# Performance work log

Hardware: AMD Instinct MI355X
Metric: run time of the kernel (lower is better)

The kernel has to match this reference:

```python
import jax, jax.numpy as jnp
import numpy as np
import math

H = 16
EPS = 1e-5

def _layernorm(x, g, b):
    mu = jnp.mean(x, axis=-1, keepdims=True)
    var = jnp.var(x, axis=-1, keepdims=True)
    return (x - mu) * jax.lax.rsqrt(var + EPS) * g + b

def setup_inputs() -> dict:
    key = jax.random.key(0)
    ks = jax.random.split(key, 8)
    B, S, D, F, M = 2, 2048, 1024, 4096, 64
    dh = D // H
    s = 1.0 / math.sqrt(D)
    return {
        "x": jax.random.normal(ks[0], (B, S, D), jnp.float32),
        "Wq": jax.random.normal(ks[1], (D, D), jnp.float32) * s,
        "Wk": jax.random.normal(ks[2], (D, D), jnp.float32) * s,
        "Wv": jax.random.normal(ks[3], (D, D), jnp.float32) * s,
        "Wo": jax.random.normal(ks[4], (D, D), jnp.float32) * s,
        "Mk": jax.random.normal(ks[5], (H, dh, M), jnp.float32) / math.sqrt(dh),
        "ln1_g": jnp.ones((D,), jnp.float32),
        "ln1_b": jnp.zeros((D,), jnp.float32),
        "ln2_g": jnp.ones((D,), jnp.float32),
        "ln2_b": jnp.zeros((D,), jnp.float32),
        "W1": jax.random.normal(ks[6], (D, F), jnp.float32) * s,
        "b1": jnp.zeros((F,), jnp.float32),
        "W2": jax.random.normal(ks[7], (F, D), jnp.float32) / math.sqrt(F),
        "b2": jnp.zeros((D,), jnp.float32),
    }

def reference(x, Wq, Wk, Wv, Wo, Mk, ln1_g, ln1_b, ln2_g, ln2_b, W1, b1, W2, b2):
    B, S, D = x.shape
    dh = D // H
    def split(t):  # (B,S,D) -> (B,H,S,dh)
        return t.reshape(B, S, H, dh).transpose(0, 2, 1, 3)
    qh = split(x @ Wq)
    kh = split(x @ Wk)
    vh = split(x @ Wv)
    q_mem = jnp.einsum('bhsd,hdm->bhsm', qh, Mk)
    k_mem = jnp.einsum('bhsd,hdm->bhsm', kh, Mk)
    attn = jnp.einsum('bhsm,bhtm->bhst', q_mem, k_mem) / math.sqrt(dh)
    attn = jax.nn.softmax(attn, axis=-1)
    ctx = jnp.einsum('bhst,bhtd->bhsd', attn, vh)
    ctx = ctx.transpose(0, 2, 1, 3).reshape(B, S, D)
    x = _layernorm(x + ctx @ Wo, ln1_g, ln1_b)
    ff = jax.nn.gelu(x @ W1 + b1, approximate=False) @ W2 + b2
    return _layernorm(x + ff, ln2_g, ln2_b)
```

## Files before the change

### kernel.cpp

```cpp
#include <hip/hip_runtime.h>
#include <math.h>

#define NH 16
#define DH 64
#define MDIM 64
#define DMODEL 1024
#define FDIM 4096
#define BATCH 2
#define SEQ 2048
#define NROWS (BATCH*SEQ)

typedef short bf16x8 __attribute__((ext_vector_type(8)));
typedef float f32x4 __attribute__((ext_vector_type(4)));

__device__ __forceinline__ float gelu_f(float v) {
    return 0.5f * v * (1.0f + erff(v * 0.70710678118654752f));
}
__device__ __forceinline__ ushort f2bf(float f) {
    union { float f; unsigned u; } v; v.f = f;
    unsigned r = v.u + 0x7fffu + ((v.u >> 16) & 1u);
    return (ushort)(r >> 16);
}
__device__ __forceinline__ float bf2f(ushort h) {
    union { unsigned u; float f; } v; v.u = ((unsigned)h) << 16;
    return v.f;
}
__device__ __forceinline__ void gl_lds16(const ushort* g, ushort* l) {
    __builtin_amdgcn_global_load_lds((const __attribute__((address_space(1))) void*)g,
                                     (__attribute__((address_space(3))) void*)l, 16, 0, 0);
}

__global__ __launch_bounds__(256)
void splitA_kernel(const float* __restrict__ X, ushort* __restrict__ hi,
                   ushort* __restrict__ lo, int n4) {
    int i = blockIdx.x * 256 + threadIdx.x;
    if (i >= n4) return;
    float4 v = ((const float4*)X)[i];
    ushort4 h, l;
    h.x = f2bf(v.x); l.x = f2bf(v.x - bf2f(h.x));
    h.y = f2bf(v.y); l.y = f2bf(v.y - bf2f(h.y));
    h.z = f2bf(v.z); l.z = f2bf(v.z - bf2f(h.z));
    h.w = f2bf(v.w); l.w = f2bf(v.w - bf2f(h.w));
    ((ushort4*)hi)[i] = h;
    ((ushort4*)lo)[i] = l;
}

__global__ __launch_bounds__(256)
void splitT_kernel(const float* __restrict__ W, ushort* __restrict__ Thi,
                   ushort* __restrict__ Tlo, int K, int N) {
    __shared__ float tile[64][65];
    const int n0 = blockIdx.x * 64;
    const int k0 = blockIdx.y * 64;
    const int t  = threadIdx.x;
    const int r  = t >> 4;
    const int c4 = (t & 15) * 4;
#pragma unroll
    for (int i = 0; i < 4; ++i) {
        int row = r + i * 16;
        float4 v = *(const float4*)&W[(size_t)(k0 + row) * N + n0 + c4];
        tile[c4 + 0][row] = v.x;
        tile[c4 + 1][row] = v.y;
        tile[c4 + 2][row] = v.z;
        tile[c4 + 3][row] = v.w;
    }
    __syncthreads();
#pragma unroll
    for (int i = 0; i < 4; ++i) {
        int row = r + i * 16;
        float a = tile[row][c4 + 0], b = tile[row][c4 + 1];
        float c = tile[row][c4 + 2], d = tile[row][c4 + 3];
        ushort4 h, l;
        h.x = f2bf(a); l.x = f2bf(a - bf2f(h.x));
        h.y = f2bf(b); l.y = f2bf(b - bf2f(h.y));
        h.z = f2bf(c); l.z = f2bf(c - bf2f(h.z));
        h.w = f2bf(d); l.w = f2bf(d - bf2f(h.w));
        size_t off = (size_t)(n0 + row) * K + k0 + c4;
        *(ushort4*)&Thi[off] = h;
        *(ushort4*)&Tlo[off] = l;
    }
}

template<int ACT, int SPLIT_OUT>
__global__ __launch_bounds__(256)
void mfma_gemm(const ushort* __restrict__ Ahi, const ushort* __restrict__ Alo,
               const ushort* __restrict__ BThi, const ushort* __restrict__ BTlo,
               const float* __restrict__ bias, float* __restrict__ C,
               ushort* __restrict__ Chi, ushort* __restrict__ Clo,
               int K, int N) {
    __shared__ ushort As[128 * 32];
    __shared__ ushort Bs[128 * 32];
    const int t    = threadIdx.x;
    const int lane = t & 63;
    const int wid  = t >> 6;
    const int wr   = wid >> 1;
    const int wc   = wid & 1;
    const int i0   = blockIdx.y * 128;
    const int n0   = blockIdx.x * 128;
    const int srow = t >> 2;
    const int scol = (t & 3) * 8;
    ushort* aDst0 = As + t * 8;
    ushort* aDst1 = As + 2048 + t * 8;
    ushort* bDst0 = Bs + t * 8;
    ushort* bDst1 = Bs + 2048 + t * 8;

    f32x4 acc[4][4];
#pragma unroll
    for (int m = 0; m < 4; ++m)
#pragma unroll
        for (int n = 0; n < 4; ++n) {
            acc[m][n][0] = 0.f; acc[m][n][1] = 0.f;
            acc[m][n][2] = 0.f; acc[m][n][3] = 0.f;
        }

    const int aOff = (wr * 64 + (lane & 15)) * 32 + (lane >> 4) * 8;
    const int bOff = (wc * 64 + (lane & 15)) * 32 + (lane >> 4) * 8;

    for (int seg = 0; seg < 3; ++seg) {
        const ushort* Ab = (seg == 1) ? Alo : Ahi;
        const ushort* Bb = (seg == 2) ? BTlo : BThi;
        const ushort* Ap0 = Ab + (size_t)(i0 + srow) * K + scol;
        const ushort* Ap1 = Ap0 + (size_t)64 * K;
        const ushort* Bp0 = Bb + (size_t)(n0 + srow) * K + scol;
        const ushort* Bp1 = Bp0 + (size_t)64 * K;
        for (int k0 = 0; k0 < K; k0 += 32) {
            __syncthreads();
            gl_lds16(Ap0 + k0, aDst0);
            gl_lds16(Ap1 + k0, aDst1);
            gl_lds16(Bp0 + k0, bDst0);
            gl_lds16(Bp1 + k0, bDst1);
            __syncthreads();
            bf16x8 af[4], bfr[4];
#pragma unroll
            for (int m = 0; m < 4; ++m)
                af[m] = *(const bf16x8*)&As[aOff + m * 16 * 32];
#pragma unroll
            for (int n = 0; n < 4; ++n)
                bfr[n] = *(const bf16x8*)&Bs[bOff + n * 16 * 32];
#pragma unroll
            for (int m = 0; m < 4; ++m)
#pragma unroll
                for (int n = 0; n < 4; ++n)
                    acc[m][n] = __builtin_amdgcn_mfma_f32_16x16x32_bf16(af[m], bfr[n], acc[m][n], 0, 0, 0);
        }
    }

    const int orow  = i0 + wr * 64 + (lane >> 4) * 4;
    const int ocol0 = n0 + wc * 64 + (lane & 15);
#pragma unroll
    for (int n = 0; n < 4; ++n) {
        const int colg = ocol0 + n * 16;
        float bv = bias ? bias[colg] : 0.f;
#pragma unroll
        for (int m = 0; m < 4; ++m) {
#pragma unroll
            for (int r = 0; r < 4; ++r) {
                const int rowg = orow + m * 16 + r;
                float v = acc[m][n][r] + bv;
                if (ACT == 1) v = gelu_f(v);
                size_t off = (size_t)rowg * N + colg;
                if (SPLIT_OUT) {
                    ushort h = f2bf(v);
                    Chi[off] = h;
                    Clo[off] = f2bf(v - bf2f(h));
                } else {
                    C[off] = v;
                }
            }
        }
    }
}

__global__ __launch_bounds__(256)
void headproj_kernel(const float* __restrict__ X, int xstride, const float* __restrict__ Mk,
                     ushort* __restrict__ oh, ushort* __restrict__ ol) {
    __shared__ float Qs[64][65];
    __shared__ float Ms[64][68];
    const int s0 = blockIdx.x * 64;
    const int h  = blockIdx.y;
    const int b  = blockIdx.z;
    const int t  = threadIdx.x;
    const int tc = t & 15, tr = t >> 4;
    const float* xb = X + (size_t)(b * SEQ + s0) * xstride + h * 64;
    const float* mk = Mk + (size_t)h * 64 * 64;
#pragma unroll
    for (int i = 0; i < 4; ++i) {
        int e4  = t + i * 256;
        int row = e4 >> 4;
        int c4  = (e4 & 15) << 2;
        float4 q4 = *(const float4*)(xb + (size_t)row * xstride + c4);
        Qs[c4 + 0][row] = q4.x;
        Qs[c4 + 1][row] = q4.y;
        Qs[c4 + 2][row] = q4.z;
        Qs[c4 + 3][row] = q4.w;
        float4 m4 = *(const float4*)(mk + row * 64 + c4);
        *(float4*)&Ms[row][c4] = m4;
    }
    __syncthreads();
    float acc[4][4] = {};
#pragma unroll 16
    for (int kk = 0; kk < 64; ++kk) {
        float a0 = Qs[kk][tr * 4 + 0];
        float a1 = Qs[kk][tr * 4 + 1];
        float a2 = Qs[kk][tr * 4 + 2];
        float a3 = Qs[kk][tr * 4 + 3];
        float4 b4 = *(const float4*)&Ms[kk][tc * 4];
        acc[0][0] += a0 * b4.x; acc[0][1] += a0 * b4.y; acc[0][2] += a0 * b4.z; acc[0][3] += a0 * b4.w;
        acc[1][0] += a1 * b4.x; acc[1][1] += a1 * b4.y; acc[1][2] += a1 * b4.z; acc[1][3] += a1 * b4.w;
        acc[2][0] += a2 * b4.x; acc[2][1] += a2 * b4.y; acc[2][2] += a2 * b4.z; acc[2][3] += a2 * b4.w;
        acc[3][0] += a3 * b4.x; acc[3][1] += a3 * b4.y; acc[3][2] += a3 * b4.z; acc[3][3] += a3 * b4.w;
    }
    ushort* oph = oh + ((size_t)(b * NH + h) * SEQ + s0) * 64;
    ushort* opl = ol + ((size_t)(b * NH + h) * SEQ + s0) * 64;
#pragma unroll
    for (int i = 0; i < 4; ++i) {
        ushort4 h4, l4;
        h4.x = f2bf(acc[i][0]); l4.x = f2bf(acc[i][0] - bf2f(h4.x));
        h4.y = f2bf(acc[i][1]); l4.y = f2bf(acc[i][1] - bf2f(h4.y));
        h4.z = f2bf(acc[i][2]); l4.z = f2bf(acc[i][2] - bf2f(h4.z));
        h4.w = f2bf(acc[i][3]); l4.w = f2bf(acc[i][3] - bf2f(h4.w));
        *(ushort4*)(oph + (size_t)(tr * 4 + i) * 64 + tc * 4) = h4;
        *(ushort4*)(opl + (size_t)(tr * 4 + i) * 64 + tc * 4) = l4;
    }
}

__global__ __launch_bounds__(256)
void vsplitT_kernel(const float* __restrict__ qkv, ushort* __restrict__ vth,
                    ushort* __restrict__ vtl) {
    __shared__ float tile[64][65];
    const int s0 = blockIdx.x * 64;
    const int h  = blockIdx.y;
    const int b  = blockIdx.z;
    const int t  = threadIdx.x;
    const int r  = t >> 4;
    const int c4 = (t & 15) * 4;
    const float* src = qkv + (size_t)(b * SEQ + s0) * 3072 + 2048 + h * 64;
#pragma unroll
    for (int i = 0; i < 4; ++i) {
        int srow = r + i * 16;
        float4 v = *(const float4*)(src + (size_t)srow * 3072 + c4);
        tile[c4 + 0][srow] = v.x;
        tile[c4 + 1][srow] = v.y;
        tile[c4 + 2][srow] = v.z;
        tile[c4 + 3][srow] = v.w;
    }
    __syncthreads();
    const size_t obase = (size_t)(b * NH + h) * 64 * SEQ + s0;
#pragma unroll
    for (int i = 0; i < 4; ++i) {
        int d = r + i * 16;
        float a = tile[d][c4 + 0], bb = tile[d][c4 + 1];
        float c = tile[d][c4 + 2], dd = tile[d][c4 + 3];
        ushort4 h4, l4;
        h4.x = f2bf(a);  l4.x = f2bf(a - bf2f(h4.x));
        h4.y = f2bf(bb); l4.y = f2bf(bb - bf2f(h4.y));
        h4.z = f2bf(c);  l4.z = f2bf(c - bf2f(h4.z));
        h4.w = f2bf(dd); l4.w = f2bf(dd - bf2f(h4.w));
        *(ushort4*)&vth[obase + (size_t)d * SEQ + c4] = h4;
        *(ushort4*)&vtl[obase + (size_t)d * SEQ + c4] = l4;
    }
}

__global__ __launch_bounds__(256)
void attn_mfma(const ushort* __restrict__ qmh, const ushort* __restrict__ qml,
               const ushort* __restrict__ kmh, const ushort* __restrict__ kml,
               const ushort* __restrict__ vth, const ushort* __restrict__ vtl,
               ushort* __restrict__ ctx_hi, ushort* __restrict__ ctx_lo) {
    __shared__ ushort pbuf[4][2][1024];
    const int q0 = blockIdx.x * 64;
    const int h  = blockIdx.y;
    const int b  = blockIdx.z;
    const int t  = threadIdx.x;
    const int lane = t & 63;
    const int w  = t >> 6;
    const int rg = lane >> 4;
    const int lc = lane & 15;
    const size_t bh = (size_t)b * NH + h;

    const ushort* qb_h = qmh + (bh * SEQ + q0 + w * 16 + lc) * 64 + rg * 8;
    const ushort* qb_l = qml + (bh * SEQ + q0 + w * 16 + lc) * 64 + rg * 8;
    bf16x8 qfh[2], qfl[2];
    qfh[0] = *(const bf16x8*)(qb_h);
    qfh[1] = *(const bf16x8*)(qb_h + 32);
    qfl[0] = *(const bf16x8*)(qb_l);
    qfl[1] = *(const bf16x8*)(qb_l + 32);

    const ushort* kb_h = kmh + (bh * SEQ + lc) * 64 + rg * 8;
    const ushort* kb_l = kml + (bh * SEQ + lc) * 64 + rg * 8;
    const ushort* vb_h = vth + (bh * 64 + lc) * SEQ + rg * 8;
    const ushort* vb_l = vtl + (bh * 64 + lc) * SEQ + rg * 8;

    f32x4 ctx[4];
#pragma unroll
    for (int n = 0; n < 4; ++n) { ctx[n][0] = 0.f; ctx[n][1] = 0.f; ctx[n][2] = 0.f; ctx[n][3] = 0.f; }
    float m_r[4] = { -INFINITY, -INFINITY, -INFINITY, -INFINITY };
    float l_r[4] = { 0.f, 0.f, 0.f, 0.f };

    ushort* ph = &pbuf[w][0][0];
    ushort* pl = &pbuf[w][1][0];

    for (int kv0 = 0; kv0 < SEQ; kv0 += 64) {
        f32x4 sacc[4];
#pragma unroll
        for (int n = 0; n < 4; ++n) { sacc[n][0] = 0.f; sacc[n][1] = 0.f; sacc[n][2] = 0.f; sacc[n][3] = 0.f; }
        bf16x8 bf[4][2];
#pragma unroll
        for (int n = 0; n < 4; ++n) {
            bf[n][0] = *(const bf16x8*)(kb_h + (size_t)(kv0 + 16 * n) * 64);
            bf[n][1] = *(const bf16x8*)(kb_h + (size_t)(kv0 + 16 * n) * 64 + 32);
        }
#pragma unroll
        for (int n = 0; n < 4; ++n) {
            sacc[n] = __builtin_amdgcn_mfma_f32_16x16x32_bf16(qfh[0], bf[n][0], sacc[n], 0, 0, 0);
            sacc[n] = __builtin_amdgcn_mfma_f32_16x16x32_bf16(qfh[1], bf[n][1], sacc[n], 0, 0, 0);
            sacc[n] = __builtin_amdgcn_mfma_f32_16x16x32_bf16(qfl[0], bf[n][0], sacc[n], 0, 0, 0);
            sacc[n] = __builtin_amdgcn_mfma_f32_16x16x32_bf16(qfl[1], bf[n][1], sacc[n], 0, 0, 0);
        }
#pragma unroll
        for (int n = 0; n < 4; ++n) {
            bf[n][0] = *(const bf16x8*)(kb_l + (size_t)(kv0 + 16 * n) * 64);
            bf[n][1] = *(const bf16x8*)(kb_l + (size_t)(kv0 + 16 * n) * 64 + 32);
        }
#pragma unroll
        for (int n = 0; n < 4; ++n) {
            sacc[n] = __builtin_amdgcn_mfma_f32_16x16x32_bf16(qfh[0], bf[n][0], sacc[n], 0, 0, 0);
            sacc[n] = __builtin_amdgcn_mfma_f32_16x16x32_bf16(qfh[1], bf[n][1], sacc[n], 0, 0, 0);
        }
#pragma unroll
        for (int r = 0; r < 4; ++r) {
            float s0 = sacc[0][r] * 0.125f;
            float s1 = sacc[1][r] * 0.125f;
            float s2 = sacc[2][r] * 0.125f;
            float s3 = sacc[3][r] * 0.125f;
            float pm = fmaxf(fmaxf(s0, s1), fmaxf(s2, s3));
            pm = fmaxf(pm, __shfl_xor(pm, 1));
            pm = fmaxf(pm, __shfl_xor(pm, 2));
            pm = fmaxf(pm, __shfl_xor(pm, 4));
            pm = fmaxf(pm, __shfl_xor(pm, 8));
            float mnew  = fmaxf(m_r[r], pm);
            float alpha = __expf(m_r[r] - mnew);
            m_r[r] = mnew;
            float p0 = __expf(s0 - mnew);
            float p1 = __expf(s1 - mnew);
            float p2 = __expf(s2 - mnew);
            float p3 = __expf(s3 - mnew);
            float rs = p0 + p1 + p2 + p3;
            rs += __shfl_xor(rs, 1);
            rs += __shfl_xor(rs, 2);
            rs += __shfl_xor(rs, 4);
            rs += __shfl_xor(rs, 8);
            l_r[r] = l_r[r] * alpha + rs;
            ctx[0][r] *= alpha; ctx[1][r] *= alpha; ctx[2][r] *= alpha; ctx[3][r] *= alpha;
            const int q = rg * 4 + r;
            const int swz = (q & 7) << 3;
            const int rowb = q * 64;
            ushort hh;
            hh = f2bf(p0); ph[(rowb + lc)      ^ swz] = hh; pl[(rowb + lc)      ^ swz] = f2bf(p0 - bf2f(hh));
            hh = f2bf(p1); ph[(rowb + lc + 16) ^ swz] = hh; pl[(rowb + lc + 16) ^ swz] = f2bf(p1 - bf2f(hh));
            hh = f2bf(p2); ph[(rowb + lc + 32) ^ swz] = hh; pl[(rowb + lc + 32) ^ swz] = f2bf(p2 - bf2f(hh));
            hh = f2bf(p3); ph[(rowb + lc + 48) ^ swz] = hh; pl[(rowb + lc + 48) ^ swz] = f2bf(p3 - bf2f(hh));
        }
        bf16x8 pah[2], pal[2];
        {
            const int swz = (lc & 7) << 3;
            pah[0] = *(const bf16x8*)&ph[(lc * 64 + rg * 8)      ^ swz];
            pah[1] = *(const bf16x8*)&ph[(lc * 64 + rg * 8 + 32) ^ swz];
            pal[0] = *(const bf16x8*)&pl[(lc * 64 + rg * 8)      ^ swz];
            pal[1] = *(const bf16x8*)&pl[(lc * 64 + rg * 8 + 32) ^ swz];
        }
#pragma unroll
        for (int n = 0; n < 4; ++n) {
            bf[n][0] = *(const bf16x8*)(vb_h + (size_t)(16 * n) * SEQ + kv0);
            bf[n][1] = *(const bf16x8*)(vb_h + (size_t)(16 * n) * SEQ + kv0 + 32);
        }
#pragma unroll
        for (int n = 0; n < 4; ++n) {
            ctx[n] = __builtin_amdgcn_mfma_f32_16x16x32_bf16(pah[0], bf[n][0], ctx[n], 0, 0, 0);
            ctx[n] = __builtin_amdgcn_mfma_f32_16x16x32_bf16(pah[1], bf[n][1], ctx[n], 0, 0, 0);
            ctx[n] = __builtin_amdgcn_mfma_f32_16x16x32_bf16(pal[0], bf[n][0], ctx[n], 0, 0, 0);
            ctx[n] = __builtin_amdgcn_mfma_f32_16x16x32_bf16(pal[1], bf[n][1], ctx[n], 0, 0, 0);
        }
#pragma unroll
        for (int n = 0; n < 4; ++n) {
            bf[n][0] = *(const bf16x8*)(vb_l + (size_t)(16 * n) * SEQ + kv0);
            bf[n][1] = *(const bf16x8*)(vb_l + (size_t)(16 * n) * SEQ + kv0 + 32);
        }
#pragma unroll
        for (int n = 0; n < 4; ++n) {
            ctx[n] = __builtin_amdgcn_mfma_f32_16x16x32_bf16(pah[0], bf[n][0], ctx[n], 0, 0, 0);
            ctx[n] = __builtin_amdgcn_mfma_f32_16x16x32_bf16(pah[1], bf[n][1], ctx[n], 0, 0, 0);
        }
    }
#pragma unroll
    for (int r = 0; r < 4; ++r) {
        float inv = 1.0f / l_r[r];
        const int q = q0 + w * 16 + rg * 4 + r;
        size_t base = ((size_t)b * SEQ + q) * DMODEL + h * 64 + lc;
#pragma unroll
        for (int n = 0; n < 4; ++n) {
            float o = ctx[n][r] * inv;
            ushort hh = f2bf(o);
            ctx_hi[base + 16 * n] = hh;
            ctx_lo[base + 16 * n] = f2bf(o - bf2f(hh));
        }
    }
}

__global__ __launch_bounds__(256)
void ln_kernel(const float* __restrict__ X, const float* __restrict__ R,
               const float* __restrict__ gw, const float* __restrict__ bw,
               float* __restrict__ out, ushort* __restrict__ ohi, ushort* __restrict__ olo) {
    __shared__ float red[8];
    const int i = blockIdx.x;
    const int t = threadIdx.x;
    const float* xp = X + (size_t)i * DMODEL;
    const float* rp = R + (size_t)i * DMODEL;
    float4 xv = *(const float4*)(xp + t * 4);
    float4 rv = *(const float4*)(rp + t * 4);
    float v0 = xv.x + rv.x, v1 = xv.y + rv.y, v2 = xv.z + rv.z, v3 = xv.w + rv.w;
    float sum = v0 + v1 + v2 + v3;
    float sq  = v0 * v0 + v1 * v1 + v2 * v2 + v3 * v3;
#pragma unroll
    for (int off = 32; off > 0; off >>= 1) {
        sum += __shfl_down(sum, off, 64);
        sq  += __shfl_down(sq,  off, 64);
    }
    int wid = t >> 6;
    if ((t & 63) == 0) { red[wid] = sum; red[4 + wid] = sq; }
    __syncthreads();
    sum = red[0] + red[1] + red[2] + red[3];
    sq  = red[4] + red[5] + red[6] + red[7];
    float mu   = sum * (1.0f / DMODEL);
    float var  = sq * (1.0f / DMODEL) - mu * mu;
    float rstd = rsqrtf(var + 1e-5f);
    float4 gv = *(const float4*)(gw + t * 4);
    float4 bv = *(const float4*)(bw + t * 4);
    float4 o;
    o.x = (v0 - mu) * rstd * gv.x + bv.x;
    o.y = (v1 - mu) * rstd * gv.y + bv.y;
    o.z = (v2 - mu) * rstd * gv.z + bv.z;
    o.w = (v3 - mu) * rstd * gv.w + bv.w;
    *(float4*)(out + (size_t)i * DMODEL + t * 4) = o;
    if (ohi) {
        ushort4 h, l;
        h.x = f2bf(o.x); l.x = f2bf(o.x - bf2f(h.x));
        h.y = f2bf(o.y); l.y = f2bf(o.y - bf2f(h.y));
        h.z = f2bf(o.z); l.z = f2bf(o.z - bf2f(h.z));
        h.w = f2bf(o.w); l.w = f2bf(o.w - bf2f(h.w));
        size_t off = (size_t)i * DMODEL + t * 4;
        *(ushort4*)&ohi[off] = h;
        *(ushort4*)&olo[off] = l;
    }
}

extern "C" void kernel_launch(void* const* d_in, const int* in_sizes, int n_in,
                              void* d_out, int out_size, void* d_ws, size_t ws_size,
                              hipStream_t stream) {
    const float* x   = (const float*)d_in[0];
    const float* Wq  = (const float*)d_in[1];
    const float* Wk  = (const float*)d_in[2];
    const float* Wv  = (const float*)d_in[3];
    const float* Wo  = (const float*)d_in[4];
    const float* Mk  = (const float*)d_in[5];
    const float* g1  = (const float*)d_in[6];
    const float* bl1 = (const float*)d_in[7];
    const float* g2  = (const float*)d_in[8];
    const float* bl2 = (const float*)d_in[9];
    const float* W1  = (const float*)d_in[10];
    const float* bf1 = (const float*)d_in[11];
    const float* W2  = (const float*)d_in[12];
    const float* bf2 = (const float*)d_in[13];
    float* out = (float*)d_out;
    char* wsb  = (char*)d_ws;

    const size_t MB = 1024 * 1024;
    float*  qkv   = (float*)(wsb + 0 * MB);
    ushort* qmh   = (ushort*)(wsb + 48 * MB);
    ushort* qml   = (ushort*)(wsb + 56 * MB);
    ushort* kmh   = (ushort*)(wsb + 64 * MB);
    ushort* kml   = (ushort*)(wsb + 72 * MB);
    ushort* vth   = (ushort*)(wsb + 80 * MB);
    ushort* vtl   = (ushort*)(wsb + 88 * MB);
    ushort* x_hi  = (ushort*)(wsb + 96 * MB);
    ushort* x_lo  = (ushort*)(wsb + 104 * MB);
    ushort* ctx_hi = x_hi;
    ushort* ctx_lo = x_lo;
    float*  wo_out = (float*)(wsb + 112 * MB);
    float*  ff2    = wo_out;
    float*  y      = (float*)(wsb + 128 * MB);
    ushort* y_hi   = (ushort*)(wsb + 144 * MB);
    ushort* y_lo   = (ushort*)(wsb + 152 * MB);
    ushort* wqkvT_hi = (ushort*)(wsb + 160 * MB);
    ushort* wqkvT_lo = (ushort*)(wsb + 166 * MB);
    ushort* woT_hi   = (ushort*)(wsb + 172 * MB);
    ushort* woT_lo   = (ushort*)(wsb + 174 * MB);
    ushort* w1T_hi   = (ushort*)(wsb + 176 * MB);
    ushort* w1T_lo   = (ushort*)(wsb + 184 * MB);
    ushort* w2T_hi   = (ushort*)(wsb + 64 * MB);
    ushort* w2T_lo   = (ushort*)(wsb + 72 * MB);
    ushort* h1_hi    = (ushort*)(wsb + 0 * MB);
    ushort* h1_lo    = (ushort*)(wsb + 32 * MB);

    dim3 blk(256);
    dim3 hgrid(SEQ / 64, NH, BATCH);
    splitT_kernel<<<dim3(16, 16), blk, 0, stream>>>(Wq, wqkvT_hi, wqkvT_lo, DMODEL, DMODEL);
    splitT_kernel<<<dim3(16, 16), blk, 0, stream>>>(Wk, wqkvT_hi + (size_t)1024 * 1024, wqkvT_lo + (size_t)1024 * 1024, DMODEL, DMODEL);
    splitT_kernel<<<dim3(16, 16), blk, 0, stream>>>(Wv, wqkvT_hi + (size_t)2048 * 1024, wqkvT_lo + (size_t)2048 * 1024, DMODEL, DMODEL);
    splitT_kernel<<<dim3(16, 16), blk, 0, stream>>>(Wo, woT_hi, woT_lo, DMODEL, DMODEL);
    splitT_kernel<<<dim3(64, 16), blk, 0, stream>>>(W1, w1T_hi, w1T_lo, DMODEL, FDIM);
    splitA_kernel<<<dim3(4096), blk, 0, stream>>>(x, x_hi, x_lo, NROWS * DMODEL / 4);
    mfma_gemm<0, 0><<<dim3(24, 32), blk, 0, stream>>>(x_hi, x_lo, wqkvT_hi, wqkvT_lo,
                                                      nullptr, qkv, nullptr, nullptr, DMODEL, 3072);
    headproj_kernel<<<hgrid, blk, 0, stream>>>(qkv + 0,    3072, Mk, qmh, qml);
    headproj_kernel<<<hgrid, blk, 0, stream>>>(qkv + 1024, 3072, Mk, kmh, kml);
    vsplitT_kernel<<<hgrid, blk, 0, stream>>>(qkv, vth, vtl);
    attn_mfma<<<hgrid, blk, 0, stream>>>(qmh, qml, kmh, kml, vth, vtl, ctx_hi, ctx_lo);
    splitT_kernel<<<dim3(16, 64), blk, 0, stream>>>(W2, w2T_hi, w2T_lo, FDIM, DMODEL);
    mfma_gemm<0, 0><<<dim3(8, 32), blk, 0, stream>>>(ctx_hi, ctx_lo, woT_hi, woT_lo,
                                                     nullptr, wo_out, nullptr, nullptr, DMODEL, DMODEL);
    ln_kernel<<<dim3(NROWS), blk, 0, stream>>>(x, wo_out, g1, bl1, y, y_hi, y_lo);
    mfma_gemm<1, 1><<<dim3(32, 32), blk, 0, stream>>>(y_hi, y_lo, w1T_hi, w1T_lo,
                                                      bf1, nullptr, h1_hi, h1_lo, DMODEL, FDIM);
    mfma_gemm<0, 0><<<dim3(8, 32), blk, 0, stream>>>(h1_hi, h1_lo, w2T_hi, w2T_lo,
                                                     bf2, ff2, nullptr, nullptr, FDIM, DMODEL);
    ln_kernel<<<dim3(NROWS), blk, 0, stream>>>(y, ff2, g2, bl2, out, nullptr, nullptr);
}
```

Measured before the change: 1.256 ms.

## Use single-wave attention blocks with register prefetch of next K tile

The attention kernel now launches one 64-thread wavefront per block, each handling 16 query rows, so the grid has four times as many blocks. Inside the KV loop the next K hi/lo tile is prefetched into registers while the current one is consumed, and V loads are issued earlier so they overlap the softmax. This aims to hide global-memory latency and raise occupancy, at the cost of more live registers and smaller blocks with less shared scheduling.

```diff
diff --git a/kernel.cpp b/kernel.cpp
--- a/kernel.cpp
+++ b/kernel.cpp
@@ -260,24 +260,23 @@
     }
 }
 
-__global__ __launch_bounds__(256)
+__global__ __launch_bounds__(64)
 void attn_mfma(const ushort* __restrict__ qmh, const ushort* __restrict__ qml,
                const ushort* __restrict__ kmh, const ushort* __restrict__ kml,
                const ushort* __restrict__ vth, const ushort* __restrict__ vtl,
                ushort* __restrict__ ctx_hi, ushort* __restrict__ ctx_lo) {
-    __shared__ ushort pbuf[4][2][1024];
-    const int q0 = blockIdx.x * 64;
+    __shared__ ushort ph[1024];
+    __shared__ ushort pl[1024];
+    const int q0 = blockIdx.x * 16;
     const int h  = blockIdx.y;
     const int b  = blockIdx.z;
-    const int t  = threadIdx.x;
-    const int lane = t & 63;
-    const int w  = t >> 6;
+    const int lane = threadIdx.x;
     const int rg = lane >> 4;
     const int lc = lane & 15;
     const size_t bh = (size_t)b * NH + h;
 
-    const ushort* qb_h = qmh + (bh * SEQ + q0 + w * 16 + lc) * 64 + rg * 8;
-    const ushort* qb_l = qml + (bh * SEQ + q0 + w * 16 + lc) * 64 + rg * 8;
+    const ushort* qb_h = qmh + (bh * SEQ + q0 + lc) * 64 + rg * 8;
+    const ushort* qb_l = qml + (bh * SEQ + q0 + lc) * 64 + rg * 8;
     bf16x8 qfh[2], qfl[2];
     qfh[0] = *(const bf16x8*)(qb_h);
     qfh[1] = *(const bf16x8*)(qb_h + 32);
@@ -295,35 +294,43 @@
     float m_r[4] = { -INFINITY, -INFINITY, -INFINITY, -INFINITY };
     float l_r[4] = { 0.f, 0.f, 0.f, 0.f };
 
-    ushort* ph = &pbuf[w][0][0];
-    ushort* pl = &pbuf[w][1][0];
+    bf16x8 kh[4][2], kl[4][2];
+#pragma unroll
+    for (int n = 0; n < 4; ++n) {
+        kh[n][0] = *(const bf16x8*)(kb_h + (size_t)(16 * n) * 64);
+        kh[n][1] = *(const bf16x8*)(kb_h + (size_t)(16 * n) * 64 + 32);
+        kl[n][0] = *(const bf16x8*)(kb_l + (size_t)(16 * n) * 64);
+        kl[n][1] = *(const bf16x8*)(kb_l + (size_t)(16 * n) * 64 + 32);
+    }
 
     for (int kv0 = 0; kv0 < SEQ; kv0 += 64) {
+        bf16x8 vh[4][2];
+#pragma unroll
+        for (int n = 0; n < 4; ++n) {
+            vh[n][0] = *(const bf16x8*)(vb_h + (size_t)(16 * n) * SEQ + kv0);
+            vh[n][1] = *(const bf16x8*)(vb_h + (size_t)(16 * n) * SEQ + kv0 + 32);
+        }
         f32x4 sacc[4];
 #pragma unroll
         for (int n = 0; n < 4; ++n) { sacc[n][0] = 0.f; sacc[n][1] = 0.f; sacc[n][2] = 0.f; sacc[n][3] = 0.f; }
-        bf16x8 bf[4][2];
-#pragma unroll
-        for (int n = 0; n < 4; ++n) {
-            bf[n][0] = *(const bf16x8*)(kb_h + (size_t)(kv0 + 16 * n) * 64);
-            bf[n][1] = *(const bf16x8*)(kb_h + (size_t)(kv0 + 16 * n) * 64 + 32);
-        }
-#pragma unroll
-        for (int n = 0; n < 4; ++n) {
-            sacc[n] = __builtin_amdgcn_mfma_f32_16x16x32_bf16(qfh[0], bf[n][0], sacc[n], 0, 0, 0);
-            sacc[n] = __builtin_amdgcn_mfma_f32_16x16x32_bf16(qfh[1], bf[n][1], sacc[n], 0, 0, 0);
-            sacc[n] = __builtin_amdgcn_mfma_f32_16x16x32_bf16(qfl[0], bf[n][0], sacc[n], 0, 0, 0);
-            sacc[n] = __builtin_amdgcn_mfma_f32_16x16x32_bf16(qfl[1], bf[n][1], sacc[n], 0, 0, 0);
-        }
-#pragma unroll
-        for (int n = 0; n < 4; ++n) {
-            bf[n][0] = *(const bf16x8*)(kb_l + (size_t)(kv0 + 16 * n) * 64);
-            bf[n][1] = *(const bf16x8*)(kb_l + (size_t)(kv0 + 16 * n) * 64 + 32);
-        }
-#pragma unroll
-        for (int n = 0; n < 4; ++n) {
-            sacc[n] = __builtin_amdgcn_mfma_f32_16x16x32_bf16(qfh[0], bf[n][0], sacc[n], 0, 0, 0);
-            sacc[n] = __builtin_amdgcn_mfma_f32_16x16x32_bf16(qfh[1], bf[n][1], sacc[n], 0, 0, 0);
+#pragma unroll
+        for (int n = 0; n < 4; ++n) {
+            sacc[n] = __builtin_amdgcn_mfma_f32_16x16x32_bf16(qfh[0], kh[n][0], sacc[n], 0, 0, 0);
+            sacc[n] = __builtin_amdgcn_mfma_f32_16x16x32_bf16(qfh[1], kh[n][1], sacc[n], 0, 0, 0);
+            sacc[n] = __builtin_amdgcn_mfma_f32_16x16x32_bf16(qfl[0], kh[n][0], sacc[n], 0, 0, 0);
+            sacc[n] = __builtin_amdgcn_mfma_f32_16x16x32_bf16(qfl[1], kh[n][1], sacc[n], 0, 0, 0);
+            sacc[n] = __builtin_amdgcn_mfma_f32_16x16x32_bf16(qfh[0], kl[n][0], sacc[n], 0, 0, 0);
+            sacc[n] = __builtin_amdgcn_mfma_f32_16x16x32_bf16(qfh[1], kl[n][1], sacc[n], 0, 0, 0);
+        }
+        if (kv0 + 64 < SEQ) {
+            const size_t nb = (size_t)(kv0 + 64) * 64;
+#pragma unroll
+            for (int n = 0; n < 4; ++n) {
+                kh[n][0] = *(const bf16x8*)(kb_h + nb + (size_t)(16 * n) * 64);
+                kh[n][1] = *(const bf16x8*)(kb_h + nb + (size_t)(16 * n) * 64 + 32);
+                kl[n][0] = *(const bf16x8*)(kb_l + nb + (size_t)(16 * n) * 64);
+                kl[n][1] = *(const bf16x8*)(kb_l + nb + (size_t)(16 * n) * 64 + 32);
+            }
         }
 #pragma unroll
         for (int r = 0; r < 4; ++r) {
@@ -359,6 +366,12 @@
             hh = f2bf(p2); ph[(rowb + lc + 32) ^ swz] = hh; pl[(rowb + lc + 32) ^ swz] = f2bf(p2 - bf2f(hh));
             hh = f2bf(p3); ph[(rowb + lc + 48) ^ swz] = hh; pl[(rowb + lc + 48) ^ swz] = f2bf(p3 - bf2f(hh));
         }
+        bf16x8 vl[4][2];
+#pragma unroll
+        for (int n = 0; n < 4; ++n) {
+            vl[n][0] = *(const bf16x8*)(vb_l + (size_t)(16 * n) * SEQ + kv0);
+            vl[n][1] = *(const bf16x8*)(vb_l + (size_t)(16 * n) * SEQ + kv0 + 32);
+        }
         bf16x8 pah[2], pal[2];
         {
             const int swz = (lc & 7) << 3;
@@ -369,31 +382,21 @@
         }
 #pragma unroll
         for (int n = 0; n < 4; ++n) {
-            bf[n][0] = *(const bf16x8*)(vb_h + (size_t)(16 * n) * SEQ + kv0);
-            bf[n][1] = *(const bf16x8*)(vb_h + (size_t)(16 * n) * SEQ + kv0 + 32);
-        }
-#pragma unroll
-        for (int n = 0; n < 4; ++n) {
-            ctx[n] = __builtin_amdgcn_mfma_f32_16x16x32_bf16(pah[0], bf[n][0], ctx[n], 0, 0, 0);
-            ctx[n] = __builtin_amdgcn_mfma_f32_16x16x32_bf16(pah[1], bf[n][1], ctx[n], 0, 0, 0);
-            ctx[n] = __builtin_amdgcn_mfma_f32_16x16x32_bf16(pal[0], bf[n][0], ctx[n], 0, 0, 0);
-            ctx[n] = __builtin_amdgcn_mfma_f32_16x16x32_bf16(pal[1], bf[n][1], ctx[n], 0, 0, 0);
-        }
-#pragma unroll
-        for (int n = 0; n < 4; ++n) {
-            bf[n][0] = *(const bf16x8*)(vb_l + (size_t)(16 * n) * SEQ + kv0);
-            bf[n][1] = *(const bf16x8*)(vb_l + (size_t)(16 * n) * SEQ + kv0 + 32);
-        }
-#pragma unroll
-        for (int n = 0; n < 4; ++n) {
-            ctx[n] = __builtin_amdgcn_mfma_f32_16x16x32_bf16(pah[0], bf[n][0], ctx[n], 0, 0, 0);
-            ctx[n] = __builtin_amdgcn_mfma_f32_16x16x32_bf16(pah[1], bf[n][1], ctx[n], 0, 0, 0);
+            ctx[n] = __builtin_amdgcn_mfma_f32_16x16x32_bf16(pah[0], vh[n][0], ctx[n], 0, 0, 0);
+            ctx[n] = __builtin_amdgcn_mfma_f32_16x16x32_bf16(pah[1], vh[n][1], ctx[n], 0, 0, 0);
+            ctx[n] = __builtin_amdgcn_mfma_f32_16x16x32_bf16(pal[0], vh[n][0], ctx[n], 0, 0, 0);
+            ctx[n] = __builtin_amdgcn_mfma_f32_16x16x32_bf16(pal[1], vh[n][1], ctx[n], 0, 0, 0);
+        }
+#pragma unroll
+        for (int n = 0; n < 4; ++n) {
+            ctx[n] = __builtin_amdgcn_mfma_f32_16x16x32_bf16(pah[0], vl[n][0], ctx[n], 0, 0, 0);
+            ctx[n] = __builtin_amdgcn_mfma_f32_16x16x32_bf16(pah[1], vl[n][1], ctx[n], 0, 0, 0);
         }
     }
 #pragma unroll
     for (int r = 0; r < 4; ++r) {
         float inv = 1.0f / l_r[r];
-        const int q = q0 + w * 16 + rg * 4 + r;
+        const int q = q0 + rg * 4 + r;
         size_t base = ((size_t)b * SEQ + q) * DMODEL + h * 64 + lc;
 #pragma unroll
         for (int n = 0; n < 4; ++n) {
@@ -513,7 +516,7 @@
     headproj_kernel<<<hgrid, blk, 0, stream>>>(qkv + 0,    3072, Mk, qmh, qml);
     headproj_kernel<<<hgrid, blk, 0, stream>>>(qkv + 1024, 3072, Mk, kmh, kml);
     vsplitT_kernel<<<hgrid, blk, 0, stream>>>(qkv, vth, vtl);
-    attn_mfma<<<hgrid, blk, 0, stream>>>(qmh, qml, kmh, kml, vth, vtl, ctx_hi, ctx_lo);
+    attn_mfma<<<dim3(SEQ / 16, NH, BATCH), dim3(64), 0, stream>>>(qmh, qml, kmh, kml, vth, vtl, ctx_hi, ctx_lo);
     splitT_kernel<<<dim3(16, 64), blk, 0, stream>>>(W2, w2T_hi, w2T_lo, FDIM, DMODEL);
     mfma_gemm<0, 0><<<dim3(8, 32), blk, 0, stream>>>(ctx_hi, ctx_lo, woT_hi, woT_lo,
                                                      nullptr, wo_out, nullptr, nullptr, DMODEL, DMODEL);
```

New measurement: 1.201 ms. 1.05x faster.
